# Kernel tuning notes

Hardware: AMD Instinct MI355X
Metric: run time of the kernel (lower is better)

## Reference

```python
import jax, jax.numpy as jnp
import numpy as np

N = 512      # n_res (act is a square pair representation [N, N, C])
C = 128      # act_dim / c_pair
I = 128      # num_intermediate_channel
EQUATION = 'ikc,jkc->ijc'  # 'outgoing' triangle multiplication
EPS = 1e-5

def _layernorm(x, g, b):
    mu = jnp.mean(x, axis=-1, keepdims=True)
    var = jnp.mean(jnp.square(x - mu), axis=-1, keepdims=True)
    return (x - mu) * jax.lax.rsqrt(var + EPS) * g + b

def setup_inputs() -> dict:
    key = jax.random.key(0)
    ks = jax.random.split(key, 12)
    s_c = 1.0 / np.sqrt(C)
    s_i = 1.0 / np.sqrt(I)
    return {
        'act': 0.1 * jax.random.normal(ks[0], (N, N, C), dtype=jnp.float32),
        'mask': (jax.random.uniform(ks[1], (N, N)) > 0.5).astype(jnp.float32),
        'ln_in_g': jnp.ones((C,), jnp.float32),
        'ln_in_b': jnp.zeros((C,), jnp.float32),
        'lp_w': s_c * jax.random.normal(ks[2], (C, I), jnp.float32),
        'lp_b': jnp.zeros((I,), jnp.float32),
        'rp_w': s_c * jax.random.normal(ks[3], (C, I), jnp.float32),
        'rp_b': jnp.zeros((I,), jnp.float32),
        'lg_w': s_c * jax.random.normal(ks[4], (C, I), jnp.float32),
        'lg_b': jnp.zeros((I,), jnp.float32),
        'rg_w': s_c * jax.random.normal(ks[5], (C, I), jnp.float32),
        'rg_b': jnp.zeros((I,), jnp.float32),
        'ln_c_g': jnp.ones((I,), jnp.float32),
        'ln_c_b': jnp.zeros((I,), jnp.float32),
        'out_w': s_i * jax.random.normal(ks[6], (I, C), jnp.float32),
        'out_b': jnp.zeros((C,), jnp.float32),
        'gate_w': s_c * jax.random.normal(ks[7], (C, C), jnp.float32),
        'gate_b': jnp.zeros((C,), jnp.float32),
    }

def reference(act, mask, ln_in_g, ln_in_b, lp_w, lp_b, rp_w, rp_b,
              lg_w, lg_b, rg_w, rg_b, ln_c_g, ln_c_b, out_w, out_b,
              gate_w, gate_b):
    m = mask[..., None]                                   # [N, N, 1]
    a = _layernorm(act, ln_in_g, ln_in_b)                 # input layernorm
    input_act = a
    # masked projections fused with sigmoid gates
    left = m * (a @ lp_w + lp_b) * jax.nn.sigmoid(a @ lg_w + lg_b)    # [N,N,I]
    right = m * (a @ rp_w + rp_b) * jax.nn.sigmoid(a @ rg_w + rg_b)   # [N,N,I]
    # triangle update: per-channel [N,N] x [N,N]^T matmul
    x = jnp.einsum(EQUATION, left, right)                 # [N,N,I]
    x = _layernorm(x, ln_c_g, ln_c_b)
    gate = jax.nn.sigmoid(input_act @ gate_w + gate_b)    # [N,N,C]
    return (x @ out_w + out_b) * gate
```

## Files before the change

### kernel.cpp

```cpp
#include <hip/hip_runtime.h>

#define NRES 512
#define N2   262144

typedef __attribute__((ext_vector_type(8))) short s16x8;
typedef __attribute__((ext_vector_type(4))) float f32x4;

__device__ __forceinline__ ushort f2bf(float x){
  union { float f; unsigned u; } v; v.f = x;
  unsigned r = (v.u + 0x7FFFu + ((v.u >> 16) & 1u)) >> 16;
  return (ushort)r;
}
__device__ __forceinline__ float bf2f(ushort h){
  union { unsigned u; float f; } v; v.u = ((unsigned)h) << 16; return v.f;
}
__device__ __forceinline__ unsigned pkbf(float lo, float hi){
  unsigned r;
  asm volatile("v_cvt_pk_bf16_f32 %0, %1, %2" : "=v"(r) : "v"(lo), "v"(hi));
  return r;
}
__device__ __forceinline__ float sigm(float x){ return 1.0f / (1.0f + __expf(-x)); }

__device__ __forceinline__ void gld_lds16(const void* g, void* lds){
  __builtin_amdgcn_global_load_lds((const __attribute__((address_space(1))) void*)g,
                                   (__attribute__((address_space(3))) void*)lds, 16, 0, 0);
}

__global__ void k0_prep(const float* __restrict__ lp, const float* __restrict__ lg,
                        const float* __restrict__ rp, const float* __restrict__ rg,
                        const float* __restrict__ gw, const float* __restrict__ ow,
                        ushort* __restrict__ Wt)
{
  const float* srcs[6] = {lp, lg, rp, rg, gw, ow};
  const float* wsrc = srcs[blockIdx.x];
  ushort* dst = Wt + blockIdx.x * 16384;
  for (int f = threadIdx.x; f < 16384; f += blockDim.x){
    int n = f >> 7, k = f & 127;
    dst[f] = f2bf(wsrc[k * 128 + n]);
  }
}

__global__ __launch_bounds__(512) void k1_proj(
    const float* __restrict__ act,  const float* __restrict__ mask,
    const float* __restrict__ ln_g, const float* __restrict__ ln_b,
    const float* __restrict__ lp_b, const float* __restrict__ lg_b,
    const float* __restrict__ rp_b, const float* __restrict__ rg_b,
    const float* __restrict__ gate_b, const ushort* __restrict__ Wt,
    ushort* __restrict__ leftg, ushort* __restrict__ rightg,
    ushort* __restrict__ gateg)
{
  __shared__ ushort Alds[128 * 136];
  __shared__ ushort Scr[8][16 * 72];
  const int t  = threadIdx.x;
  const int p0 = blockIdx.x * 128;
  const int lane = t & 63, w = t >> 6;
  const int cl = lane & 15, h = lane >> 4;
  const int c  = w * 16 + cl;

  s16x8 wf[5][4];
  #pragma unroll
  for (int m5 = 0; m5 < 5; ++m5)
    #pragma unroll
    for (int ks = 0; ks < 4; ++ks)
      wf[m5][ks] = *(const s16x8*)(Wt + (size_t)m5 * 16384 + (size_t)c * 128 + ks * 32 + h * 8);
  const float pb_l = lp_b[c], gb_l = lg_b[c];
  const float pb_r = rp_b[c], gb_r = rg_b[c];
  const float gb_g = gate_b[c];

  {
    const int g = t >> 5, j = t & 31;
    const float4 gv = *(const float4*)(ln_g + j * 4);
    const float4 bv = *(const float4*)(ln_b + j * 4);
    #pragma unroll
    for (int i = 0; i < 8; ++i){
      const int r = g + (i << 4);
      float4 v = *(const float4*)(act + (size_t)(p0 + r) * 128 + j * 4);
      float s = v.x + v.y + v.z + v.w;
      float q = v.x*v.x + v.y*v.y + v.z*v.z + v.w*v.w;
      #pragma unroll
      for (int m = 1; m < 32; m <<= 1){ s += __shfl_xor(s, m); q += __shfl_xor(q, m); }
      float mu = s * (1.0f / 128.0f);
      float rs = rsqrtf(q * (1.0f / 128.0f) - mu * mu + 1e-5f);
      uint2 o;
      o.x = pkbf((v.x - mu) * rs * gv.x + bv.x, (v.y - mu) * rs * gv.y + bv.y);
      o.y = pkbf((v.z - mu) * rs * gv.z + bv.z, (v.w - mu) * rs * gv.w + bv.w);
      *(uint2*)&Alds[r * 136 + j * 4] = o;
    }
  }
  __syncthreads();

  ushort* scr = &Scr[w][0];
  const int rc = lane >> 2, rq = lane & 3;
  const f32x4 z = {0.f, 0.f, 0.f, 0.f};

  #pragma unroll
  for (int mh = 0; mh < 2; ++mh){
    s16x8 a[4][4];
    #pragma unroll
    for (int m = 0; m < 4; ++m)
      #pragma unroll
      for (int ks = 0; ks < 4; ++ks)
        a[m][ks] = *(const s16x8*)&Alds[(mh*64 + m*16 + cl) * 136 + ks*32 + h*8];

    float mk[4][4];
    #pragma unroll
    for (int m = 0; m < 4; ++m)
      #pragma unroll
      for (int r = 0; r < 4; ++r)
        mk[m][r] = mask[p0 + mh*64 + m*16 + h*4 + r];

    auto wv_store = [&](const uint2 v[4], ushort* dstg){
      #pragma unroll
      for (int m = 0; m < 4; ++m)
        *(uint2*)&scr[cl * 72 + m * 16 + h * 4] = v[m];
      asm volatile("s_waitcnt lgkmcnt(0)" ::: "memory");
      s16x8 r0 = *(const s16x8*)&scr[rc * 72 + rq * 16];
      s16x8 r1 = *(const s16x8*)&scr[rc * 72 + rq * 16 + 8];
      *(s16x8*)(dstg + (size_t)rc * N2 + rq * 16)     = r0;
      *(s16x8*)(dstg + (size_t)rc * N2 + rq * 16 + 8) = r1;
    };
    const size_t doff = (size_t)(w * 16) * N2 + p0 + mh * 64;

    {
      f32x4 accP[4], accG[4];
      #pragma unroll
      for (int m = 0; m < 4; ++m){ accP[m] = z; accG[m] = z; }
      #pragma unroll
      for (int ks = 0; ks < 4; ++ks)
        #pragma unroll
        for (int m = 0; m < 4; ++m){
          accP[m] = __builtin_amdgcn_mfma_f32_16x16x32_bf16(a[m][ks], wf[0][ks], accP[m], 0, 0, 0);
          accG[m] = __builtin_amdgcn_mfma_f32_16x16x32_bf16(a[m][ks], wf[1][ks], accG[m], 0, 0, 0);
        }
      uint2 o[4];
      #pragma unroll
      for (int m = 0; m < 4; ++m){
        float x0 = mk[m][0] * (accP[m][0] + pb_l) * sigm(accG[m][0] + gb_l);
        float x1 = mk[m][1] * (accP[m][1] + pb_l) * sigm(accG[m][1] + gb_l);
        float x2 = mk[m][2] * (accP[m][2] + pb_l) * sigm(accG[m][2] + gb_l);
        float x3 = mk[m][3] * (accP[m][3] + pb_l) * sigm(accG[m][3] + gb_l);
        o[m].x = pkbf(x0, x1); o[m].y = pkbf(x2, x3);
      }
      wv_store(o, leftg + doff);
    }
    {
      f32x4 accP[4], accG[4];
      #pragma unroll
      for (int m = 0; m < 4; ++m){ accP[m] = z; accG[m] = z; }
      #pragma unroll
      for (int ks = 0; ks < 4; ++ks)
        #pragma unroll
        for (int m = 0; m < 4; ++m){
          accP[m] = __builtin_amdgcn_mfma_f32_16x16x32_bf16(a[m][ks], wf[2][ks], accP[m], 0, 0, 0);
          accG[m] = __builtin_amdgcn_mfma_f32_16x16x32_bf16(a[m][ks], wf[3][ks], accG[m], 0, 0, 0);
        }
      uint2 o[4];
      #pragma unroll
      for (int m = 0; m < 4; ++m){
        float x0 = mk[m][0] * (accP[m][0] + pb_r) * sigm(accG[m][0] + gb_r);
        float x1 = mk[m][1] * (accP[m][1] + pb_r) * sigm(accG[m][1] + gb_r);
        float x2 = mk[m][2] * (accP[m][2] + pb_r) * sigm(accG[m][2] + gb_r);
        float x3 = mk[m][3] * (accP[m][3] + pb_r) * sigm(accG[m][3] + gb_r);
        o[m].x = pkbf(x0, x1); o[m].y = pkbf(x2, x3);
      }
      wv_store(o, rightg + doff);
    }
    {
      f32x4 acc[4];
      #pragma unroll
      for (int m = 0; m < 4; ++m) acc[m] = z;
      #pragma unroll
      for (int ks = 0; ks < 4; ++ks)
        #pragma unroll
        for (int m = 0; m < 4; ++m)
          acc[m] = __builtin_amdgcn_mfma_f32_16x16x32_bf16(a[m][ks], wf[4][ks], acc[m], 0, 0, 0);
      uint2 o[4];
      #pragma unroll
      for (int m = 0; m < 4; ++m){
        o[m].x = pkbf(sigm(acc[m][0] + gb_g), sigm(acc[m][1] + gb_g));
        o[m].y = pkbf(sigm(acc[m][2] + gb_g), sigm(acc[m][3] + gb_g));
      }
      wv_store(o, gateg + doff);
    }
  }
}

__global__ __launch_bounds__(256) void k2_tri(const ushort* __restrict__ leftg,
                                              const ushort* __restrict__ rightg,
                                              ushort* __restrict__ X)
{
  __shared__ ushort Ab[2][128 * 32];
  __shared__ ushort Bb[2][128 * 32];
  const int t = threadIdx.x, lane = t & 63, w = t >> 6;
  const int b = blockIdx.x;
  const int c = b & 127, tile = b >> 7;
  const int tm = (tile >> 2) * 128, tn = (tile & 3) * 128;
  const char* Lc = (const char*)(leftg  + (size_t)c * N2);
  const char* Rc = (const char*)(rightg + (size_t)c * N2);
  ushort* Xc = X + (size_t)c * N2;
  const int wr = w >> 1, wc = w & 1, cl = lane & 15, h = lane >> 4;

  const int o0 = (w    ) * 1024 + lane * 16;
  const int o1 = (w + 4) * 1024 + lane * 16;
  const int row0 = o0 >> 6, row1 = o1 >> 6;
  const int sk0 = ((((o0 >> 4) & 3) ^ (row0 & 3)) << 4);
  const int sk1 = ((((o1 >> 4) & 3) ^ (row1 & 3)) << 4);

  f32x4 acc[4][4];
  const f32x4 z = {0.f, 0.f, 0.f, 0.f};
  #pragma unroll
  for (int m = 0; m < 4; ++m)
    #pragma unroll
    for (int n = 0; n < 4; ++n) acc[m][n] = z;

  auto stage = [&](int buf, int kt){
    gld_lds16(Lc + (size_t)(tm + row0) * 1024 + kt * 64 + sk0, (char*)&Ab[buf][0] + o0);
    gld_lds16(Lc + (size_t)(tm + row1) * 1024 + kt * 64 + sk1, (char*)&Ab[buf][0] + o1);
    gld_lds16(Rc + (size_t)(tn + row0) * 1024 + kt * 64 + sk0, (char*)&Bb[buf][0] + o0);
    gld_lds16(Rc + (size_t)(tn + row1) * 1024 + kt * 64 + sk1, (char*)&Bb[buf][0] + o1);
  };
  const int rsw = ((h ^ (cl & 3)) << 4);
  auto compute = [&](int buf){
    s16x8 a2[4], b2[4];
    #pragma unroll
    for (int m = 0; m < 4; ++m)
      a2[m] = *(const s16x8*)((const char*)&Ab[buf][0] + (wr*64 + m*16 + cl) * 64 + rsw);
    #pragma unroll
    for (int n = 0; n < 4; ++n)
      b2[n] = *(const s16x8*)((const char*)&Bb[buf][0] + (wc*64 + n*16 + cl) * 64 + rsw);
    #pragma unroll
    for (int m = 0; m < 4; ++m)
      #pragma unroll
      for (int n = 0; n < 4; ++n)
        acc[m][n] = __builtin_amdgcn_mfma_f32_16x16x32_bf16(a2[m], b2[n], acc[m][n], 0, 0, 0);
  };

  stage(0, 0);
  __syncthreads();
  int cur = 0;
  for (int kt = 0; kt < 15; ++kt){
    stage(cur ^ 1, kt + 1);
    compute(cur);
    __syncthreads();
    cur ^= 1;
  }
  compute(cur);

  #pragma unroll
  for (int m = 0; m < 4; ++m)
    #pragma unroll
    for (int n = 0; n < 4; ++n)
      #pragma unroll
      for (int r = 0; r < 4; ++r)
        Xc[(size_t)(tm + wr*64 + m*16 + h*4 + r) * NRES + tn + wc*64 + n*16 + cl] =
            f2bf(acc[m][n][r]);
}

__global__ __launch_bounds__(256) void k3_out(
    const ushort* __restrict__ X, const ushort* __restrict__ gateg,
    const ushort* __restrict__ Wt5,
    const float* __restrict__ ln_g, const float* __restrict__ ln_b,
    const float* __restrict__ ob, float* __restrict__ out)
{
  __shared__ ushort Alds[128 * 136];
  __shared__ ushort Wlds[128 * 136];
  __shared__ float part[8][2][128];
  __shared__ float stat[2][128];
  const int t = threadIdx.x;
  const int p0 = blockIdx.x * 128;
  const int g = t >> 5, j = t & 31;

  float4 xv[16];
  float s0 = 0, s1 = 0, s2 = 0, s3 = 0, q0 = 0, q1 = 0, q2 = 0, q3 = 0;
  #pragma unroll
  for (int i = 0; i < 16; ++i){
    const int cch = g + (i << 3);
    ushort4 u4 = *(const ushort4*)(X + (size_t)cch * N2 + p0 + j * 4);
    xv[i].x = bf2f(u4.x); xv[i].y = bf2f(u4.y);
    xv[i].z = bf2f(u4.z); xv[i].w = bf2f(u4.w);
    s0 += xv[i].x; q0 += xv[i].x * xv[i].x;
    s1 += xv[i].y; q1 += xv[i].y * xv[i].y;
    s2 += xv[i].z; q2 += xv[i].z * xv[i].z;
    s3 += xv[i].w; q3 += xv[i].w * xv[i].w;
  }
  part[g][0][j*4+0] = s0; part[g][0][j*4+1] = s1;
  part[g][0][j*4+2] = s2; part[g][0][j*4+3] = s3;
  part[g][1][j*4+0] = q0; part[g][1][j*4+1] = q1;
  part[g][1][j*4+2] = q2; part[g][1][j*4+3] = q3;
  __syncthreads();
  if (t < 128){
    float s = 0, q = 0;
    #pragma unroll
    for (int gg = 0; gg < 8; ++gg){ s += part[gg][0][t]; q += part[gg][1][t]; }
    float mu = s * (1.0f / 128.0f);
    float rs = rsqrtf(q * (1.0f / 128.0f) - mu * mu + 1e-5f);
    stat[0][t] = mu; stat[1][t] = rs;
  }
  __syncthreads();
  #pragma unroll
  for (int i = 0; i < 16; ++i){
    const int cch = g + (i << 3);
    const float gc = ln_g[cch], bc = ln_b[cch];
    const int p = j * 4;
    Alds[(p+0) * 136 + cch] = f2bf((xv[i].x - stat[0][p+0]) * stat[1][p+0] * gc + bc);
    Alds[(p+1) * 136 + cch] = f2bf((xv[i].y - stat[0][p+1]) * stat[1][p+1] * gc + bc);
    Alds[(p+2) * 136 + cch] = f2bf((xv[i].z - stat[0][p+2]) * stat[1][p+2] * gc + bc);
    Alds[(p+3) * 136 + cch] = f2bf((xv[i].w - stat[0][p+3]) * stat[1][p+3] * gc + bc);
  }
  #pragma unroll
  for (int u = 0; u < 8; ++u){
    int f = t + u * 256;
    int n = f >> 4, k8 = f & 15;
    *(s16x8*)&Wlds[n * 136 + k8 * 8] = *(const s16x8*)(Wt5 + f * 8);
  }
  __syncthreads();

  const int lane = t & 63, w = t >> 6;
  const int wr = w >> 1, wc = w & 1, cl = lane & 15, h = lane >> 4;
  f32x4 acc[4][4];
  const f32x4 z = {0.f, 0.f, 0.f, 0.f};
  #pragma unroll
  for (int m = 0; m < 4; ++m)
    #pragma unroll
    for (int n = 0; n < 4; ++n) acc[m][n] = z;
  #pragma unroll
  for (int ks = 0; ks < 4; ++ks){
    s16x8 a[4], bfr[4];
    #pragma unroll
    for (int m = 0; m < 4; ++m)
      a[m] = *(const s16x8*)&Alds[(wr*64 + m*16 + cl) * 136 + ks*32 + h*8];
    #pragma unroll
    for (int n = 0; n < 4; ++n)
      bfr[n] = *(const s16x8*)&Wlds[(wc*64 + n*16 + cl) * 136 + ks*32 + h*8];
    #pragma unroll
    for (int m = 0; m < 4; ++m)
      #pragma unroll
      for (int n = 0; n < 4; ++n)
        acc[m][n] = __builtin_amdgcn_mfma_f32_16x16x32_bf16(a[m], bfr[n], acc[m][n], 0, 0, 0);
  }

  float obv[4];
  #pragma unroll
  for (int n = 0; n < 4; ++n) obv[n] = ob[wc*64 + n*16 + cl];
  #pragma unroll
  for (int m = 0; m < 4; ++m)
    #pragma unroll
    for (int n = 0; n < 4; ++n){
      const int cc = wc*64 + n*16 + cl;
      ushort4 g4 = *(const ushort4*)(gateg + (size_t)cc * N2 + p0 + wr*64 + m*16 + h*4);
      const size_t pbase = p0 + wr*64 + m*16 + h*4;
      out[(pbase+0) * 128 + cc] = (acc[m][n][0] + obv[n]) * bf2f(g4.x);
      out[(pbase+1) * 128 + cc] = (acc[m][n][1] + obv[n]) * bf2f(g4.y);
      out[(pbase+2) * 128 + cc] = (acc[m][n][2] + obv[n]) * bf2f(g4.z);
      out[(pbase+3) * 128 + cc] = (acc[m][n][3] + obv[n]) * bf2f(g4.w);
    }
}

extern "C" void kernel_launch(void* const* d_in, const int* in_sizes, int n_in,
                              void* d_out, int out_size, void* d_ws, size_t ws_size,
                              hipStream_t stream)
{
  const float* act    = (const float*)d_in[0];
  const float* mask   = (const float*)d_in[1];
  const float* ln_in_g = (const float*)d_in[2];
  const float* ln_in_b = (const float*)d_in[3];
  const float* lp_w = (const float*)d_in[4];
  const float* lp_b = (const float*)d_in[5];
  const float* rp_w = (const float*)d_in[6];
  const float* rp_b = (const float*)d_in[7];
  const float* lg_w = (const float*)d_in[8];
  const float* lg_b = (const float*)d_in[9];
  const float* rg_w = (const float*)d_in[10];
  const float* rg_b = (const float*)d_in[11];
  const float* ln_c_g = (const float*)d_in[12];
  const float* ln_c_b = (const float*)d_in[13];
  const float* out_w  = (const float*)d_in[14];
  const float* out_b  = (const float*)d_in[15];
  const float* gate_w = (const float*)d_in[16];
  const float* gate_b = (const float*)d_in[17];
  float* outp = (float*)d_out;

  char* ws = (char*)d_ws;
  ushort* Wt     = (ushort*)(ws);
  ushort* leftg  = (ushort*)(ws + 196608);
  ushort* rightg = (ushort*)(ws + 196608 + 67108864ull);
  ushort* gateg  = (ushort*)(ws + 196608 + 2ull * 67108864ull);
  ushort* X      = (ushort*)(ws + 196608 + 3ull * 67108864ull);

  k0_prep<<<dim3(6), dim3(256), 0, stream>>>(lp_w, lg_w, rp_w, rg_w, gate_w, out_w, Wt);
  k1_proj<<<dim3(2048), dim3(512), 0, stream>>>(act, mask, ln_in_g, ln_in_b,
                                                lp_b, lg_b, rp_b, rg_b, gate_b,
                                                Wt, leftg, rightg, gateg);
  k2_tri<<<dim3(2048), dim3(256), 0, stream>>>(leftg, rightg, X);
  k3_out<<<dim3(2048), dim3(256), 0, stream>>>(X, gateg, Wt + 5 * 16384,
                                               ln_c_g, ln_c_b, out_b, outp);
}
```

Before: 514.6 us.

## Split input layernorm kernel, restructure projection slabs, triple-buffer triangle matmul

```diff
diff --git a/kernel.cpp b/kernel.cpp
--- a/kernel.cpp
+++ b/kernel.cpp
@@ -25,6 +25,8 @@
   __builtin_amdgcn_global_load_lds((const __attribute__((address_space(1))) void*)g,
                                    (__attribute__((address_space(3))) void*)lds, 16, 0, 0);
 }
+
+#define VMCNT(n) asm volatile("s_waitcnt vmcnt(" #n ")" ::: "memory")
 
 __global__ void k0_prep(const float* __restrict__ lp, const float* __restrict__ lg,
                         const float* __restrict__ rp, const float* __restrict__ rg,
@@ -40,55 +42,48 @@
   }
 }
 
-__global__ __launch_bounds__(512) void k1_proj(
-    const float* __restrict__ act,  const float* __restrict__ mask,
-    const float* __restrict__ ln_g, const float* __restrict__ ln_b,
+__global__ __launch_bounds__(256) void k1a_ln(
+    const float* __restrict__ act, const float* __restrict__ ln_g,
+    const float* __restrict__ ln_b, ushort* __restrict__ a_ln)
+{
+  const int t = threadIdx.x;
+  const int p0 = blockIdx.x * 128;
+  const int g = t >> 5, j = t & 31;
+  const float4 gv = *(const float4*)(ln_g + j * 4);
+  const float4 bv = *(const float4*)(ln_b + j * 4);
+  #pragma unroll
+  for (int i = 0; i < 16; ++i){
+    const int row = p0 + g + (i << 3);
+    float4 v = *(const float4*)(act + (size_t)row * 128 + j * 4);
+    float s = v.x + v.y + v.z + v.w;
+    float q = v.x*v.x + v.y*v.y + v.z*v.z + v.w*v.w;
+    #pragma unroll
+    for (int m = 1; m < 32; m <<= 1){ s += __shfl_xor(s, m); q += __shfl_xor(q, m); }
+    float mu = s * (1.0f / 128.0f);
+    float rs = rsqrtf(q * (1.0f / 128.0f) - mu * mu + 1e-5f);
+    uint2 o;
+    o.x = pkbf((v.x - mu) * rs * gv.x + bv.x, (v.y - mu) * rs * gv.y + bv.y);
+    o.y = pkbf((v.z - mu) * rs * gv.z + bv.z, (v.w - mu) * rs * gv.w + bv.w);
+    *(uint2*)(a_ln + (size_t)row * 128 + j * 4) = o;
+  }
+}
+
+__global__ __launch_bounds__(256) void k1b_proj(
+    const ushort* __restrict__ a_ln, const float* __restrict__ mask,
     const float* __restrict__ lp_b, const float* __restrict__ lg_b,
     const float* __restrict__ rp_b, const float* __restrict__ rg_b,
     const float* __restrict__ gate_b, const ushort* __restrict__ Wt,
     ushort* __restrict__ leftg, ushort* __restrict__ rightg,
     ushort* __restrict__ gateg)
 {
-  __shared__ ushort Alds[128 * 136];
-  __shared__ ushort Scr[8][16 * 72];
-  const int t  = threadIdx.x;
+  __shared__ ushort Scr[4][16 * 72];
+  const int t = threadIdx.x;
   const int p0 = blockIdx.x * 128;
   const int lane = t & 63, w = t >> 6;
   const int cl = lane & 15, h = lane >> 4;
-  const int c  = w * 16 + cl;
-
-  s16x8 wf[5][4];
-  #pragma unroll
-  for (int m5 = 0; m5 < 5; ++m5)
-    #pragma unroll
-    for (int ks = 0; ks < 4; ++ks)
-      wf[m5][ks] = *(const s16x8*)(Wt + (size_t)m5 * 16384 + (size_t)c * 128 + ks * 32 + h * 8);
-  const float pb_l = lp_b[c], gb_l = lg_b[c];
-  const float pb_r = rp_b[c], gb_r = rg_b[c];
-  const float gb_g = gate_b[c];
-
-  {
-    const int g = t >> 5, j = t & 31;
-    const float4 gv = *(const float4*)(ln_g + j * 4);
-    const float4 bv = *(const float4*)(ln_b + j * 4);
-    #pragma unroll
-    for (int i = 0; i < 8; ++i){
-      const int r = g + (i << 4);
-      float4 v = *(const float4*)(act + (size_t)(p0 + r) * 128 + j * 4);
-      float s = v.x + v.y + v.z + v.w;
-      float q = v.x*v.x + v.y*v.y + v.z*v.z + v.w*v.w;
-      #pragma unroll
-      for (int m = 1; m < 32; m <<= 1){ s += __shfl_xor(s, m); q += __shfl_xor(q, m); }
-      float mu = s * (1.0f / 128.0f);
-      float rs = rsqrtf(q * (1.0f / 128.0f) - mu * mu + 1e-5f);
-      uint2 o;
-      o.x = pkbf((v.x - mu) * rs * gv.x + bv.x, (v.y - mu) * rs * gv.y + bv.y);
-      o.y = pkbf((v.z - mu) * rs * gv.z + bv.z, (v.w - mu) * rs * gv.w + bv.w);
-      *(uint2*)&Alds[r * 136 + j * 4] = o;
-    }
-  }
-  __syncthreads();
-
+  const float* Pb[3] = {lp_b, rp_b, gate_b};
+  const float* Gb[2] = {lg_b, rg_b};
+  ushort* dsts[3] = {leftg, rightg, gateg};
   ushort* scr = &Scr[w][0];
   const int rc = lane >> 2, rq = lane & 3;
   const f32x4 z = {0.f, 0.f, 0.f, 0.f};
@@ -100,8 +95,8 @@
     for (int m = 0; m < 4; ++m)
       #pragma unroll
       for (int ks = 0; ks < 4; ++ks)
-        a[m][ks] = *(const s16x8*)&Alds[(mh*64 + m*16 + cl) * 136 + ks*32 + h*8];
-
+        a[m][ks] = *(const s16x8*)(a_ln + (size_t)(p0 + mh*64 + m*16 + cl) * 128
+                                        + ks*32 + h*8);
     float mk[4][4];
     #pragma unroll
     for (int m = 0; m < 4; ++m)
@@ -109,78 +104,65 @@
       for (int r = 0; r < 4; ++r)
         mk[m][r] = mask[p0 + mh*64 + m*16 + h*4 + r];
 
-    auto wv_store = [&](const uint2 v[4], ushort* dstg){
+    for (int i = 0; i < 6; ++i){
+      const int slab = w * 6 + i;
+      const int out = slab >> 3;
+      const int c0 = (slab & 7) << 4;
+      const bool hasG = (out < 2);
+      const ushort* WPp = Wt + (size_t)(out * 2) * 16384 + (size_t)(c0 + cl) * 128;
+      s16x8 wfP[4], wfG[4];
+      #pragma unroll
+      for (int ks = 0; ks < 4; ++ks)
+        wfP[ks] = *(const s16x8*)(WPp + ks*32 + h*8);
+      if (hasG)
+        #pragma unroll
+        for (int ks = 0; ks < 4; ++ks)
+          wfG[ks] = *(const s16x8*)(WPp + 16384 + ks*32 + h*8);
+      const float pb = Pb[out][c0 + cl];
+      const float gb = hasG ? Gb[out][c0 + cl] : 0.f;
+
+      f32x4 accP[4], accG[4];
+      #pragma unroll
+      for (int m = 0; m < 4; ++m){ accP[m] = z; accG[m] = z; }
+      #pragma unroll
+      for (int ks = 0; ks < 4; ++ks)
+        #pragma unroll
+        for (int m = 0; m < 4; ++m)
+          accP[m] = __builtin_amdgcn_mfma_f32_16x16x32_bf16(a[m][ks], wfP[ks], accP[m], 0, 0, 0);
+      if (hasG){
+        #pragma unroll
+        for (int ks = 0; ks < 4; ++ks)
+          #pragma unroll
+          for (int m = 0; m < 4; ++m)
+            accG[m] = __builtin_amdgcn_mfma_f32_16x16x32_bf16(a[m][ks], wfG[ks], accG[m], 0, 0, 0);
+      }
+
+      uint2 o[4];
+      if (hasG){
+        #pragma unroll
+        for (int m = 0; m < 4; ++m){
+          float x0 = mk[m][0] * (accP[m][0] + pb) * sigm(accG[m][0] + gb);
+          float x1 = mk[m][1] * (accP[m][1] + pb) * sigm(accG[m][1] + gb);
+          float x2 = mk[m][2] * (accP[m][2] + pb) * sigm(accG[m][2] + gb);
+          float x3 = mk[m][3] * (accP[m][3] + pb) * sigm(accG[m][3] + gb);
+          o[m].x = pkbf(x0, x1); o[m].y = pkbf(x2, x3);
+        }
+      } else {
+        #pragma unroll
+        for (int m = 0; m < 4; ++m){
+          o[m].x = pkbf(sigm(accP[m][0] + pb), sigm(accP[m][1] + pb));
+          o[m].y = pkbf(sigm(accP[m][2] + pb), sigm(accP[m][3] + pb));
+        }
+      }
       #pragma unroll
       for (int m = 0; m < 4; ++m)
-        *(uint2*)&scr[cl * 72 + m * 16 + h * 4] = v[m];
+        *(uint2*)&scr[cl * 72 + m * 16 + h * 4] = o[m];
       asm volatile("s_waitcnt lgkmcnt(0)" ::: "memory");
+      ushort* dstg = dsts[out] + (size_t)c0 * N2 + p0 + mh * 64;
       s16x8 r0 = *(const s16x8*)&scr[rc * 72 + rq * 16];
       s16x8 r1 = *(const s16x8*)&scr[rc * 72 + rq * 16 + 8];
       *(s16x8*)(dstg + (size_t)rc * N2 + rq * 16)     = r0;
       *(s16x8*)(dstg + (size_t)rc * N2 + rq * 16 + 8) = r1;
-    };
-    const size_t doff = (size_t)(w * 16) * N2 + p0 + mh * 64;
-
-    {
-      f32x4 accP[4], accG[4];
-      #pragma unroll
-      for (int m = 0; m < 4; ++m){ accP[m] = z; accG[m] = z; }
-      #pragma unroll
-      for (int ks = 0; ks < 4; ++ks)
-        #pragma unroll
-        for (int m = 0; m < 4; ++m){
-          accP[m] = __builtin_amdgcn_mfma_f32_16x16x32_bf16(a[m][ks], wf[0][ks], accP[m], 0, 0, 0);
-          accG[m] = __builtin_amdgcn_mfma_f32_16x16x32_bf16(a[m][ks], wf[1][ks], accG[m], 0, 0, 0);
-        }
-      uint2 o[4];
-      #pragma unroll
-      for (int m = 0; m < 4; ++m){
-        float x0 = mk[m][0] * (accP[m][0] + pb_l) * sigm(accG[m][0] + gb_l);
-        float x1 = mk[m][1] * (accP[m][1] + pb_l) * sigm(accG[m][1] + gb_l);
-        float x2 = mk[m][2] * (accP[m][2] + pb_l) * sigm(accG[m][2] + gb_l);
-        float x3 = mk[m][3] * (accP[m][3] + pb_l) * sigm(accG[m][3] + gb_l);
-        o[m].x = pkbf(x0, x1); o[m].y = pkbf(x2, x3);
-      }
-      wv_store(o, leftg + doff);
-    }
-    {
-      f32x4 accP[4], accG[4];
-      #pragma unroll
-      for (int m = 0; m < 4; ++m){ accP[m] = z; accG[m] = z; }
-      #pragma unroll
-      for (int ks = 0; ks < 4; ++ks)
-        #pragma unroll
-        for (int m = 0; m < 4; ++m){
-          accP[m] = __builtin_amdgcn_mfma_f32_16x16x32_bf16(a[m][ks], wf[2][ks], accP[m], 0, 0, 0);
-          accG[m] = __builtin_amdgcn_mfma_f32_16x16x32_bf16(a[m][ks], wf[3][ks], accG[m], 0, 0, 0);
-        }
-      uint2 o[4];
-      #pragma unroll
-      for (int m = 0; m < 4; ++m){
-        float x0 = mk[m][0] * (accP[m][0] + pb_r) * sigm(accG[m][0] + gb_r);
-        float x1 = mk[m][1] * (accP[m][1] + pb_r) * sigm(accG[m][1] + gb_r);
-        float x2 = mk[m][2] * (accP[m][2] + pb_r) * sigm(accG[m][2] + gb_r);
-        float x3 = mk[m][3] * (accP[m][3] + pb_r) * sigm(accG[m][3] + gb_r);
-        o[m].x = pkbf(x0, x1); o[m].y = pkbf(x2, x3);
-      }
-      wv_store(o, rightg + doff);
-    }
-    {
-      f32x4 acc[4];
-      #pragma unroll
-      for (int m = 0; m < 4; ++m) acc[m] = z;
-      #pragma unroll
-      for (int ks = 0; ks < 4; ++ks)
-        #pragma unroll
-        for (int m = 0; m < 4; ++m)
-          acc[m] = __builtin_amdgcn_mfma_f32_16x16x32_bf16(a[m][ks], wf[4][ks], acc[m], 0, 0, 0);
-      uint2 o[4];
-      #pragma unroll
-      for (int m = 0; m < 4; ++m){
-        o[m].x = pkbf(sigm(acc[m][0] + gb_g), sigm(acc[m][1] + gb_g));
-        o[m].y = pkbf(sigm(acc[m][2] + gb_g), sigm(acc[m][3] + gb_g));
-      }
-      wv_store(o, gateg + doff);
     }
   }
 }
@@ -189,8 +171,8 @@
                                               const ushort* __restrict__ rightg,
                                               ushort* __restrict__ X)
 {
-  __shared__ ushort Ab[2][128 * 32];
-  __shared__ ushort Bb[2][128 * 32];
+  __shared__ ushort Ab[3][128 * 32];
+  __shared__ ushort Bb[3][128 * 32];
   const int t = threadIdx.x, lane = t & 63, w = t >> 6;
   const int b = blockIdx.x;
   const int c = b & 127, tile = b >> 7;
@@ -203,8 +185,8 @@
   const int o0 = (w    ) * 1024 + lane * 16;
   const int o1 = (w + 4) * 1024 + lane * 16;
   const int row0 = o0 >> 6, row1 = o1 >> 6;
-  const int sk0 = ((((o0 >> 4) & 3) ^ (row0 & 3)) << 4);
-  const int sk1 = ((((o1 >> 4) & 3) ^ (row1 & 3)) << 4);
+  const int sk0 = ((((o0 >> 4) & 3) ^ ((row0 >> 1) & 3)) << 4);
+  const int sk1 = ((((o1 >> 4) & 3) ^ ((row1 >> 1) & 3)) << 4);
 
   f32x4 acc[4][4];
   const f32x4 z = {0.f, 0.f, 0.f, 0.f};
@@ -219,7 +201,7 @@
     gld_lds16(Rc + (size_t)(tn + row0) * 1024 + kt * 64 + sk0, (char*)&Bb[buf][0] + o0);
     gld_lds16(Rc + (size_t)(tn + row1) * 1024 + kt * 64 + sk1, (char*)&Bb[buf][0] + o1);
   };
-  const int rsw = ((h ^ (cl & 3)) << 4);
+  const int rsw = ((h ^ ((cl >> 1) & 3)) << 4);
   auto compute = [&](int buf){
     s16x8 a2[4], b2[4];
     #pragma unroll
@@ -236,14 +218,25 @@
   };
 
   stage(0, 0);
-  __syncthreads();
+  stage(1, 1);
   int cur = 0;
-  for (int kt = 0; kt < 15; ++kt){
-    stage(cur ^ 1, kt + 1);
+  for (int kt = 0; kt < 14; ++kt){
+    VMCNT(4);
+    __builtin_amdgcn_s_barrier();
+    __builtin_amdgcn_sched_barrier(0);
     compute(cur);
-    __syncthreads();
-    cur ^= 1;
-  }
+    int nb = cur + 2; if (nb >= 3) nb -= 3;
+    stage(nb, kt + 2);
+    cur = (cur == 2) ? 0 : cur + 1;
+  }
+  VMCNT(4);
+  __builtin_amdgcn_s_barrier();
+  __builtin_amdgcn_sched_barrier(0);
+  compute(cur);
+  cur = (cur == 2) ? 0 : cur + 1;
+  VMCNT(0);
+  __builtin_amdgcn_s_barrier();
+  __builtin_amdgcn_sched_barrier(0);
   compute(cur);
 
   #pragma unroll
@@ -382,15 +375,17 @@
 
   char* ws = (char*)d_ws;
   ushort* Wt     = (ushort*)(ws);
-  ushort* leftg  = (ushort*)(ws + 196608);
-  ushort* rightg = (ushort*)(ws + 196608 + 67108864ull);
-  ushort* gateg  = (ushort*)(ws + 196608 + 2ull * 67108864ull);
-  ushort* X      = (ushort*)(ws + 196608 + 3ull * 67108864ull);
+  ushort* a_ln   = (ushort*)(ws + 196608);
+  ushort* leftg  = (ushort*)(ws + 196608 + 1ull * 67108864ull);
+  ushort* rightg = (ushort*)(ws + 196608 + 2ull * 67108864ull);
+  ushort* gateg  = (ushort*)(ws + 196608 + 3ull * 67108864ull);
+  ushort* X      = (ushort*)(ws + 196608 + 4ull * 67108864ull);
 
   k0_prep<<<dim3(6), dim3(256), 0, stream>>>(lp_w, lg_w, rp_w, rg_w, gate_w, out_w, Wt);
-  k1_proj<<<dim3(2048), dim3(512), 0, stream>>>(act, mask, ln_in_g, ln_in_b,
-                                                lp_b, lg_b, rp_b, rg_b, gate_b,
-                                                Wt, leftg, rightg, gateg);
+  k1a_ln<<<dim3(2048), dim3(256), 0, stream>>>(act, ln_in_g, ln_in_b, a_ln);
+  k1b_proj<<<dim3(2048), dim3(256), 0, stream>>>(a_ln, mask,
+                                                 lp_b, lg_b, rp_b, rg_b, gate_b,
+                                                 Wt, leftg, rightg, gateg);
   k2_tri<<<dim3(2048), dim3(256), 0, stream>>>(leftg, rightg, X);
   k3_out<<<dim3(2048), dim3(256), 0, stream>>>(X, gateg, Wt + 5 * 16384,
                                                ln_c_g, ln_c_b, out_b, outp);
```

New measurement: 539.3 us. 4.8% more time.
